# Optimization experiments

Measured on AMD Instinct MI355X. Metric: run time of the kernel, lower is better.

## Reference

```python
import jax, jax.numpy as jnp
import numpy as np

BN_EPS = 1e-6


def _conv1x1(x, w, b):
    # x: (B, Cin, N, K), w: (Cout, Cin), b: (Cout,)
    return jnp.einsum('oc,bcnk->bonk', w, x) + b[None, :, None, None]


def _bn(x, gamma, beta, mean, var):
    # inference-mode BatchNorm2d over channel axis 1
    inv = gamma / jnp.sqrt(var + BN_EPS)
    return x * inv[None, :, None, None] + (beta - mean * inv)[None, :, None, None]


def setup_inputs() -> dict:
    key = jax.random.key(0)
    ks = jax.random.split(key, 12)
    B, N, K = 4, 16384, 16
    C_out = 32
    C_img = 2 * C_out - 10          # 54, so concat has 2*C_out = 64 channels
    C_in1 = 2 * C_out               # 64
    C_in2 = 2 * (C_out + 3)         # 70

    points = jax.random.normal(ks[0], (B, N, 3), jnp.float32)
    image_features = jax.random.normal(ks[1], (B, C_img, N, K), jnp.float32)
    dist = jax.random.uniform(ks[2], (B, N, K), jnp.float32)
    idx = jax.random.randint(ks[3], (B, N, K), 0, N, dtype=jnp.int32)

    w1 = jax.random.normal(ks[4], (C_out, C_in1), jnp.float32) / np.sqrt(C_in1).astype(np.float32)
    b1 = jnp.zeros((C_out,), jnp.float32)
    gamma1 = jnp.ones((C_out,), jnp.float32)
    beta1 = jnp.zeros((C_out,), jnp.float32)
    mean1 = 0.1 * jax.random.normal(ks[5], (C_out,), jnp.float32)
    var1 = 0.5 + jax.random.uniform(ks[6], (C_out,), jnp.float32)

    w2 = jax.random.normal(ks[7], (C_out, C_in2), jnp.float32) / np.sqrt(C_in2).astype(np.float32)
    b2 = jnp.zeros((C_out,), jnp.float32)
    gamma2 = jnp.ones((C_out,), jnp.float32)
    beta2 = jnp.zeros((C_out,), jnp.float32)
    mean2 = 0.1 * jax.random.normal(ks[8], (C_out,), jnp.float32)
    var2 = 0.5 + jax.random.uniform(ks[9], (C_out,), jnp.float32)

    return {
        'points': points, 'image_features': image_features, 'dist': dist, 'idx': idx,
        'w1': w1, 'b1': b1, 'gamma1': gamma1, 'beta1': beta1, 'mean1': mean1, 'var1': var1,
        'w2': w2, 'b2': b2, 'gamma2': gamma2, 'beta2': beta2, 'mean2': mean2, 'var2': var2,
    }


def reference(points, image_features, dist, idx,
              w1, b1, gamma1, beta1, mean1, var1,
              w2, b2, gamma2, beta2, mean2, var2):
    B, N, K = idx.shape
    pts = jnp.swapaxes(points, 1, 2)                       # (B, 3, N)
    ep = jnp.broadcast_to(pts[:, :, :, None], (B, 3, N, K))  # extended points
    # KNN gather: nb[b, c, n, k] = pts[b, c, idx[b, n, k]]
    nb = jax.vmap(lambda p, i: p[:, i])(pts, idx)          # (B, 3, N, K)

    concat = jnp.concatenate(
        [ep, nb, ep - nb, dist[:, None, :, :], image_features], axis=1)  # (B, 64, N, K)

    h = jax.nn.relu(_bn(_conv1x1(concat, w1, b1), gamma1, beta1, mean1, var1))  # (B, 32, N, K)
    feat = jnp.concatenate([h, ep], axis=1)                # (B, 35, N, K)

    pooled = jnp.concatenate(
        [jnp.max(feat, axis=-1, keepdims=True),
         jnp.mean(feat, axis=-1, keepdims=True)], axis=1)  # (B, 70, N, 1)

    out = jax.nn.relu(_bn(_conv1x1(pooled, w2, b2), gamma2, beta2, mean2, var2))  # (B, 32, N, 1)
    return out
```

## Files before the change

### kernel.cpp

```cpp
#include <hip/hip_runtime.h>
#include <cmath>

#define BN_EPS 1e-6f
constexpr int B_     = 4;
constexpr int N_     = 16384;
constexpr int K_     = 16;
constexpr int C_IMG  = 54;
constexpr int C1     = 64;
constexpr int CO     = 32;
constexpr int C2     = 70;
constexpr int NT     = 16;
constexpr int HPAD   = 17;
constexpr int PPAD   = 76;

__global__ __launch_bounds__(256, 4) void pif_fused_kernel(
    const float* __restrict__ points,
    const float* __restrict__ imgf,
    const float* __restrict__ dist,
    const int*   __restrict__ idx,
    const float* __restrict__ w1,
    const float* __restrict__ b1,
    const float* __restrict__ g1,
    const float* __restrict__ be1,
    const float* __restrict__ m1,
    const float* __restrict__ v1,
    const float* __restrict__ w2,
    const float* __restrict__ b2,
    const float* __restrict__ g2,
    const float* __restrict__ be2,
    const float* __restrict__ m2,
    const float* __restrict__ v2,
    float* __restrict__ out)
{
    __shared__ float h_lds[CO][NT * HPAD];
    __shared__ float pooled[NT][PPAD];

    const int t    = threadIdx.x;
    const int tpb  = N_ / NT;
    const int b    = blockIdx.x / tpb;
    const int n0   = (blockIdx.x % tpb) * NT;

    const int k    = t & 15;
    const int ln   = t >> 4;
    const int n    = n0 + ln;

    float x[C1];

    const int pbase = (b * N_ + n) * 3;
    const float px = points[pbase + 0];
    const float py = points[pbase + 1];
    const float pz = points[pbase + 2];

    const int j  = idx[(b * N_ + n) * K_ + k];
    const int qb = (b * N_ + j) * 3;
    const float qx = points[qb + 0];
    const float qy = points[qb + 1];
    const float qz = points[qb + 2];

    x[0] = px;      x[1] = py;      x[2] = pz;
    x[3] = qx;      x[4] = qy;      x[5] = qz;
    x[6] = px - qx; x[7] = py - qy; x[8] = pz - qz;
    x[9] = dist[(b * N_ + n) * K_ + k];

    {
        const float* p = imgf + ((b * C_IMG) * N_ + n) * K_ + k;
        #pragma unroll
        for (int c = 0; c < C_IMG; ++c)
            x[10 + c] = p[c * (N_ * K_)];
    }

    #pragma unroll 2
    for (int o = 0; o < CO; ++o) {
        const float* wr = w1 + o * C1;
        float a0 = 0.f, a1 = 0.f;
        #pragma unroll
        for (int c = 0; c < C1; c += 2) {
            a0 = fmaf(wr[c],     x[c],     a0);
            a1 = fmaf(wr[c + 1], x[c + 1], a1);
        }
        const float acc = a0 + a1;
        const float inv = g1[o] * rsqrtf(v1[o] + BN_EPS);
        float hv = (acc + b1[o]) * inv + (be1[o] - m1[o] * inv);
        hv = fmaxf(hv, 0.f);
        h_lds[o][ln * HPAD + k] = hv;
    }
    __syncthreads();

    #pragma unroll
    for (int r = 0; r < 2; ++r) {
        const int nn = t & 15;
        const int c  = (t >> 4) + r * 16;
        float mx = 0.f;
        float sm = 0.f;
        #pragma unroll
        for (int kk = 0; kk < K_; ++kk) {
            const float v = h_lds[c][nn * HPAD + kk];
            mx = fmaxf(mx, v);
            sm += v;
        }
        pooled[nn][c]      = mx;
        pooled[nn][35 + c] = sm * (1.f / 16.f);
    }
    if (t < 48) {
        const int nn = t & 15;
        const int jj = t >> 4;
        const float v = points[(b * N_ + n0 + nn) * 3 + jj];
        pooled[nn][32 + jj] = v;
        pooled[nn][67 + jj] = v;
    }
    __syncthreads();

    #pragma unroll
    for (int r = 0; r < 2; ++r) {
        const int nn = t & 15;
        const int o  = (t >> 4) + r * 16;
        const float* wr = w2 + o * C2;
        float a0 = 0.f, a1 = 0.f;
        #pragma unroll
        for (int c = 0; c < C2; c += 2) {
            a0 = fmaf(wr[c],     pooled[nn][c],     a0);
            a1 = fmaf(wr[c + 1], pooled[nn][c + 1], a1);
        }
        const float acc = a0 + a1;
        const float inv = g2[o] * rsqrtf(v2[o] + BN_EPS);
        float ov = (acc + b2[o]) * inv + (be2[o] - m2[o] * inv);
        ov = fmaxf(ov, 0.f);
        out[(b * CO + o) * N_ + n0 + nn] = ov;
    }
}

extern "C" void kernel_launch(void* const* d_in, const int* in_sizes, int n_in,
                              void* d_out, int out_size, void* d_ws, size_t ws_size,
                              hipStream_t stream) {
    const float* points = (const float*)d_in[0];
    const float* imgf   = (const float*)d_in[1];
    const float* dist   = (const float*)d_in[2];
    const int*   idx    = (const int*)  d_in[3];
    const float* w1     = (const float*)d_in[4];
    const float* b1     = (const float*)d_in[5];
    const float* g1     = (const float*)d_in[6];
    const float* be1    = (const float*)d_in[7];
    const float* m1     = (const float*)d_in[8];
    const float* v1     = (const float*)d_in[9];
    const float* w2     = (const float*)d_in[10];
    const float* b2     = (const float*)d_in[11];
    const float* g2     = (const float*)d_in[12];
    const float* be2    = (const float*)d_in[13];
    const float* m2     = (const float*)d_in[14];
    const float* v2     = (const float*)d_in[15];
    float* out          = (float*)d_out;

    const int blocks = B_ * (N_ / NT);
    pif_fused_kernel<<<blocks, 256, 0, stream>>>(
        points, imgf, dist, idx,
        w1, b1, g1, be1, m1, v1,
        w2, b2, g2, be2, m2, v2, out);
}
```

Measured before the change: 408.3 us.

## Stream image channels in chunks into per-output accumulators instead of full input vector

The first conv is restructured from a per-output dot over a 64-float input array into 32 output accumulators updated as image-feature channels are loaded in chunks of six. This reduces the live input registers and interleaves global loads with FMA work, aiming to relieve register pressure and hide load latency. It trades that for 32 live accumulators and a fully unrolled loop. The BN epilogues also become a single fmaf each.

```diff
diff --git a/kernel.cpp b/kernel.cpp
--- a/kernel.cpp
+++ b/kernel.cpp
@@ -12,6 +12,8 @@
 constexpr int NT     = 16;
 constexpr int HPAD   = 17;
 constexpr int PPAD   = 76;
+constexpr int NK     = N_ * K_;
+constexpr int CHUNK  = 6;
 
 __global__ __launch_bounds__(256, 4) void pif_fused_kernel(
     const float* __restrict__ points,
@@ -44,43 +46,58 @@
     const int ln   = t >> 4;
     const int n    = n0 + ln;
 
-    float x[C1];
+    const int   base_nk = (b * N_ + n) * K_ + k;
+    const int   j  = idx[base_nk];
+    const float dv = dist[base_nk];
 
     const int pbase = (b * N_ + n) * 3;
     const float px = points[pbase + 0];
     const float py = points[pbase + 1];
     const float pz = points[pbase + 2];
-
-    const int j  = idx[(b * N_ + n) * K_ + k];
     const int qb = (b * N_ + j) * 3;
     const float qx = points[qb + 0];
     const float qy = points[qb + 1];
     const float qz = points[qb + 2];
 
-    x[0] = px;      x[1] = py;      x[2] = pz;
-    x[3] = qx;      x[4] = qy;      x[5] = qz;
-    x[6] = px - qx; x[7] = py - qy; x[8] = pz - qz;
-    x[9] = dist[(b * N_ + n) * K_ + k];
+    float g[10];
+    g[0] = px;      g[1] = py;      g[2] = pz;
+    g[3] = qx;      g[4] = qy;      g[5] = qz;
+    g[6] = px - qx; g[7] = py - qy; g[8] = pz - qz;
+    g[9] = dv;
 
-    {
-        const float* p = imgf + ((b * C_IMG) * N_ + n) * K_ + k;
-        #pragma unroll
-        for (int c = 0; c < C_IMG; ++c)
-            x[10 + c] = p[c * (N_ * K_)];
-    }
-
-    #pragma unroll 2
+    float acc[CO];
+    #pragma unroll
     for (int o = 0; o < CO; ++o) {
         const float* wr = w1 + o * C1;
         float a0 = 0.f, a1 = 0.f;
         #pragma unroll
-        for (int c = 0; c < C1; c += 2) {
-            a0 = fmaf(wr[c],     x[c],     a0);
-            a1 = fmaf(wr[c + 1], x[c + 1], a1);
+        for (int c = 0; c < 10; c += 2) {
+            a0 = fmaf(wr[c],     g[c],     a0);
+            a1 = fmaf(wr[c + 1], g[c + 1], a1);
         }
-        const float acc = a0 + a1;
+        acc[o] = a0 + a1;
+    }
+
+    const float* ip = imgf + (size_t)b * C_IMG * NK + (n * K_ + k);
+    #pragma unroll
+    for (int c0 = 0; c0 < C_IMG; c0 += CHUNK) {
+        float xv[CHUNK];
+        #pragma unroll
+        for (int jj = 0; jj < CHUNK; ++jj)
+            xv[jj] = ip[(c0 + jj) * NK];
+        #pragma unroll
+        for (int o = 0; o < CO; ++o) {
+            const float* wr = w1 + o * C1 + 10 + c0;
+            #pragma unroll
+            for (int jj = 0; jj < CHUNK; ++jj)
+                acc[o] = fmaf(wr[jj], xv[jj], acc[o]);
+        }
+    }
+
+    #pragma unroll
+    for (int o = 0; o < CO; ++o) {
         const float inv = g1[o] * rsqrtf(v1[o] + BN_EPS);
-        float hv = (acc + b1[o]) * inv + (be1[o] - m1[o] * inv);
+        float hv = fmaf(acc[o] + b1[o], inv, be1[o] - m1[o] * inv);
         hv = fmaxf(hv, 0.f);
         h_lds[o][ln * HPAD + k] = hv;
     }
@@ -121,9 +138,9 @@
             a0 = fmaf(wr[c],     pooled[nn][c],     a0);
             a1 = fmaf(wr[c + 1], pooled[nn][c + 1], a1);
         }
-        const float acc = a0 + a1;
+        const float acc2 = a0 + a1;
         const float inv = g2[o] * rsqrtf(v2[o] + BN_EPS);
-        float ov = (acc + b2[o]) * inv + (be2[o] - m2[o] * inv);
+        float ov = fmaf(acc2 + b2[o], inv, be2[o] - m2[o] * inv);
         ov = fmaxf(ov, 0.f);
         out[(b * CO + o) * N_ + n0 + nn] = ov;
     }
```

New measurement: 400.4 us. Within noise of the previous version (-1.9%).
